# Optimization experiments

Measured on AMD Instinct MI355X. Metric: run time of the kernel, lower is better.

## Reference

```python
import jax, jax.numpy as jnp
import numpy as np

H = 8          # num_heads
L = 256        # lifting_dim
DH = L // H    # head dim


def setup_inputs() -> dict:
    key = jax.random.key(0)
    ks = jax.random.split(key, 32)
    B, N, E = 4, 16384, 65536
    Dn, De, Dg = 128, 64, 32

    def lin_w(k, din, dout):
        return jax.random.normal(k, (din, dout), jnp.float32) * (din ** -0.5)

    inp = {
        "node_features": jax.random.normal(ks[0], (B, N, Dn), jnp.float32),
        "edge_features": jax.random.normal(ks[1], (B, E, De), jnp.float32),
        "energy": jax.random.normal(ks[2], (Dg,), jnp.float32),
        "W_node": lin_w(ks[3], Dn, L), "b_node": jnp.zeros((L,), jnp.float32),
        "W_edge": lin_w(ks[4], De, L), "b_edge": jnp.zeros((L,), jnp.float32),
        "W_graph": lin_w(ks[5], Dg, L), "b_graph": jnp.zeros((L,), jnp.float32),
        "Wq": lin_w(ks[6], L, L), "bq": jnp.zeros((L,), jnp.float32),
        # stacked per-hetero-type key/value projections: [3, L, L]
        "Wk": jnp.stack([lin_w(ks[7 + i], L, L) for i in range(3)]),
        "bk": jnp.zeros((3, L), jnp.float32),
        "Wv": jnp.stack([lin_w(ks[10 + i], L, L) for i in range(3)]),
        "bv": jnp.zeros((3, L), jnp.float32),
        "W_out": lin_w(ks[13], L, L), "b_out": jnp.zeros((L,), jnp.float32),
    }
    return inp


def _heads(x, B, T):
    # [B,T,L] -> [B,H,T,DH]
    return x.reshape(B, T, H, DH).transpose(0, 2, 1, 3)


def reference(node_features, edge_features, energy,
              W_node, b_node, W_edge, b_edge, W_graph, b_graph,
              Wq, bq, Wk, bk, Wv, bv, W_out, b_out):
    B, N, _ = node_features.shape
    lifted_nodes = node_features @ W_node + b_node            # [B,N,L]
    lifted_edges = edge_features @ W_edge + b_edge            # [B,E,L]
    lifted_graph = jnp.broadcast_to(energy, (B, 1, energy.shape[0])) @ W_graph + b_graph  # [B,1,L]

    hetero = [lifted_nodes, lifted_edges, lifted_graph]

    q = _heads(lifted_nodes @ Wq + bq, B, N)                  # [B,H,N,DH]
    q = jax.nn.softmax(q, axis=-1)

    out = None
    # NOTE: faithful to the original, `out` is overwritten each iteration,
    # so only the last hetero feature (graph) determines the output.
    for i in range(3):
        h = hetero[i]
        T = h.shape[1]
        k = jax.nn.softmax(_heads(h @ Wk[i] + bk[i], B, T), axis=-1)  # [B,H,T,DH]
        v = _heads(h @ Wv[i] + bv[i], B, T)                           # [B,H,T,DH]
        k_sum = k.sum(axis=-2, keepdims=True)                          # [B,H,1,DH]
        d_inv = 1.0 / jnp.clip((q * k_sum).sum(axis=-1, keepdims=True), 1e-8)  # [B,H,N,1]
        kv = jnp.einsum("bhtd,bhte->bhde", k, v)                       # [B,H,DH,DH]
        out = q + jnp.einsum("bhnd,bhde->bhne", q, kv) * d_inv         # [B,H,N,DH]

    out = out.transpose(0, 2, 1, 3).reshape(B, N, L)
    return out @ W_out + b_out
```

## Files before the change

kernel.cpp:

```cpp
#include <hip/hip_runtime.h>
#include <hip/hip_bf16.h>
#include <cstdint>
#include <cstddef>


typedef __attribute__((ext_vector_type(8))) short short8;
typedef __attribute__((ext_vector_type(4))) short short4v;
typedef __attribute__((ext_vector_type(4))) float floatx4;

using bf16 = __hip_bfloat16;

static constexpr int Mrows = 65536;
static constexpr int Lcols = 256;

static __device__ __forceinline__ short f2bs(float x) {
  bf16 h = __float2bfloat16(x);
  return *reinterpret_cast<short*>(&h);
}

__global__ void k_setup(const float* __restrict__ W_node,
                        const float* __restrict__ Wq,
                        const float* __restrict__ W_out,
                        const float* __restrict__ energy,
                        const float* __restrict__ W_graph,
                        const float* __restrict__ b_graph,
                        const float* __restrict__ Wk,
                        const float* __restrict__ bk,
                        const float* __restrict__ Wv,
                        const float* __restrict__ bv,
                        const float* __restrict__ b_node,
                        const float* __restrict__ bq,
                        short* __restrict__ wnq_t,
                        short* __restrict__ wto_t,
                        float* __restrict__ vvec,
                        float* __restrict__ bnq) {
  const int b = blockIdx.x;
  const int t = threadIdx.x;

  if (b < 256) {
    __shared__ float wqc[256];
    const int j = b;
    wqc[t] = Wq[t * 256 + j];
    __syncthreads();
    if (t < 128) {
      const float* wr = W_node + t * 256;
      float acc = 0.f;
#pragma unroll 8
      for (int l = 0; l < 256; ++l) acc += wr[l] * wqc[l];
      wnq_t[j * 128 + t] = f2bs(acc);
    }
  } else if (b < 512) {
    const int r = b - 256;
    wto_t[t * 256 + r] = f2bs(W_out[r * 256 + t]);
  } else {
    __shared__ float ev[32];
    __shared__ float lg[256];
    __shared__ float r1[256], r2[256];
    const int h = b - 512;
    if (t < 32) ev[t] = energy[t];
    __syncthreads();

    {
      float lgd = b_graph[t];
#pragma unroll
      for (int e = 0; e < 32; ++e) lgd += ev[e] * W_graph[e * 256 + t];
      lg[t] = lgd;
    }
    __syncthreads();

    const int g = t >> 5;
    const int c = t & 31;
    const int j = h * 32 + c;
    float p1 = 0.f, p2 = 0.f;
#pragma unroll
    for (int i = 0; i < 32; ++i) {
      const int d = g * 32 + i;
      p1 += lg[d] * Wv[2 * 65536 + d * 256 + j];
      p2 += b_node[d] * Wq[d * 256 + j];
    }
    r1[t] = p1; r2[t] = p2;
    __syncthreads();
    if (t < 32) {
      float s1 = 0.f, s2 = 0.f;
#pragma unroll
      for (int gg = 0; gg < 8; ++gg) {
        s1 += r1[gg * 32 + c]; s2 += r2[gg * 32 + c];
      }
      vvec[j] = s1 + bv[512 + j];
      bnq[j]  = s2 + bq[j];
    }
  }
}

__global__ __launch_bounds__(256, 2)
void k_fused(const float* __restrict__ nf,
             const short* __restrict__ wnq,
             const short* __restrict__ wto,
             const float* __restrict__ bnq,
             const float* __restrict__ vvec,
             const float* __restrict__ b_out,
             float* __restrict__ out) {
  constexpr int AS_STR = 136;
  constexpr int PS_STR = 264;
  constexpr int FO_STR = 260;
  __shared__ short smem[64 * PS_STR];
  float* fsm = (float*)smem;

  const int t = threadIdx.x;
  const int lane = t & 63;
  const int l15 = lane & 15;
  const int lhi = lane >> 4;
  const int cw = (t >> 6) * 64;
  const int rowBase = blockIdx.x * 64;
  const int colq = cw + lhi * 4;

  const short* wb1 = wnq + (cw + l15) * 128 + lhi * 8;
  const short* wb2 = wto + (cw + l15) * 256 + lhi * 8;

  {
    const int row = t >> 2;
    const int c0 = (t & 3) << 5;
    const float* src = nf + (size_t)(rowBase + row) * 128 + c0;
    short tmp[32];
#pragma unroll
    for (int i = 0; i < 8; ++i) {
      float4 f = *(const float4*)(src + i * 4);
      tmp[i * 4 + 0] = f2bs(f.x); tmp[i * 4 + 1] = f2bs(f.y);
      tmp[i * 4 + 2] = f2bs(f.z); tmp[i * 4 + 3] = f2bs(f.w);
    }
#pragma unroll
    for (int i = 0; i < 4; ++i)
      *(short8*)(&smem[row * AS_STR + c0 + i * 8]) = *(short8*)(&tmp[i * 8]);
  }

  short8 pbf1[4][4];
#pragma unroll
  for (int kc = 0; kc < 4; ++kc)
#pragma unroll
    for (int n = 0; n < 4; ++n)
      pbf1[kc][n] = *(const short8*)(wb1 + n * 16 * 128 + kc * 32);

  __syncthreads();

  floatx4 acc[4][4];
#pragma unroll
  for (int m = 0; m < 4; ++m)
#pragma unroll
    for (int n = 0; n < 4; ++n) acc[m][n] = (floatx4){0.f, 0.f, 0.f, 0.f};

  {
#pragma unroll
    for (int kc = 0; kc < 4; ++kc) {
      short8 af[4];
#pragma unroll
      for (int m = 0; m < 4; ++m)
        af[m] = *(const short8*)(&smem[(m * 16 + l15) * AS_STR + kc * 32 + lhi * 8]);
#pragma unroll
      for (int m = 0; m < 4; ++m)
#pragma unroll
        for (int n = 0; n < 4; ++n)
          acc[m][n] = __builtin_amdgcn_mfma_f32_16x16x32_bf16(pbf1[kc][n], af[m],
                                                              acc[m][n], 0, 0, 0);
    }
  }

  short8 pbf2[2][4];
#pragma unroll
  for (int kc = 0; kc < 2; ++kc)
#pragma unroll
    for (int n = 0; n < 4; ++n)
      pbf2[kc][n] = *(const short8*)(wb2 + n * 16 * 256 + kc * 32);
  floatx4 bnq4[4], vv4[4];
#pragma unroll
  for (int n = 0; n < 4; ++n) {
    bnq4[n] = *(const floatx4*)(&bnq[colq + n * 16]);
    vv4[n]  = *(const floatx4*)(&vvec[colq + n * 16]);
  }

  __syncthreads();

#pragma unroll
  for (int m = 0; m < 4; ++m) {
#pragma unroll
    for (int tt = 0; tt < 2; ++tt) {
      const int n0 = 2 * tt, n1 = n0 + 1;
      float e0[4], e1[4];
#pragma unroll
      for (int r = 0; r < 4; ++r) {
        e0[r] = __expf(acc[m][n0][r] + bnq4[n0][r]);
        e1[r] = __expf(acc[m][n1][r] + bnq4[n1][r]);
      }
      float s = ((e0[0] + e0[1]) + (e0[2] + e0[3]))
              + ((e1[0] + e1[1]) + (e1[2] + e1[3]));
      s += __shfl_xor(s, 16);
      s += __shfl_xor(s, 32);
      const float inv = 1.0f / s;
      short4v p0, p1;
#pragma unroll
      for (int r = 0; r < 4; ++r) {
        p0[r] = f2bs(e0[r] * inv + vv4[n0][r]);
        p1[r] = f2bs(e1[r] * inv + vv4[n1][r]);
      }
      const int prow = (m * 16 + l15) * PS_STR;
      *(short4v*)(&smem[prow + colq + n0 * 16]) = p0;
      *(short4v*)(&smem[prow + colq + n1 * 16]) = p1;
    }
  }
  floatx4 bo4[4];
#pragma unroll
  for (int n = 0; n < 4; ++n) bo4[n] = *(const floatx4*)(&b_out[colq + n * 16]);
#pragma unroll
  for (int m = 0; m < 4; ++m)
#pragma unroll
    for (int n = 0; n < 4; ++n) acc[m][n] = bo4[n];
  __syncthreads();

  {
#pragma unroll
    for (int kc = 0; kc < 8; ++kc) {
      short8 af[4], bfv[4];
#pragma unroll
      for (int n = 0; n < 4; ++n)
        bfv[n] = (kc < 2) ? pbf2[kc][n]
                          : *(const short8*)(wb2 + n * 16 * 256 + kc * 32);
#pragma unroll
      for (int m = 0; m < 4; ++m)
        af[m] = *(const short8*)(&smem[(m * 16 + l15) * PS_STR + kc * 32 + lhi * 8]);
#pragma unroll
      for (int m = 0; m < 4; ++m)
#pragma unroll
        for (int n = 0; n < 4; ++n)
          acc[m][n] = __builtin_amdgcn_mfma_f32_16x16x32_bf16(bfv[n], af[m],
                                                              acc[m][n], 0, 0, 0);
    }
  }

#pragma unroll
  for (int c = 0; c < 2; ++c) {
    __syncthreads();
#pragma unroll
    for (int mm = 0; mm < 2; ++mm) {
      const int m = c * 2 + mm;
      const int frow = (mm * 16 + l15) * FO_STR;
#pragma unroll
      for (int n = 0; n < 4; ++n)
        *(floatx4*)(&fsm[frow + colq + n * 16]) = acc[m][n];
    }
    __syncthreads();
#pragma unroll
    for (int i = 0; i < 8; ++i) {
      const int f = i * 256 + t;
      const int row = f >> 6;
      const int c4 = (f & 63) << 2;
      float4 vv = *(const float4*)(&fsm[row * FO_STR + c4]);
      *(float4*)(&out[(size_t)(rowBase + c * 32 + row) * Lcols + c4]) = vv;
    }
  }
}

extern "C" void kernel_launch(void* const* d_in, const int* in_sizes, int n_in,
                              void* d_out, int out_size, void* d_ws, size_t ws_size,
                              hipStream_t stream) {
  const float* node_features = (const float*)d_in[0];
  const float* energy  = (const float*)d_in[2];
  const float* W_node  = (const float*)d_in[3];
  const float* b_node  = (const float*)d_in[4];
  const float* W_graph = (const float*)d_in[7];
  const float* b_graph = (const float*)d_in[8];
  const float* Wq      = (const float*)d_in[9];
  const float* bq      = (const float*)d_in[10];
  const float* Wk      = (const float*)d_in[11];
  const float* bk      = (const float*)d_in[12];
  const float* Wv      = (const float*)d_in[13];
  const float* bv      = (const float*)d_in[14];
  const float* W_out   = (const float*)d_in[15];
  const float* b_out   = (const float*)d_in[16];

  char* ws = (char*)d_ws;
  short* wnq_t = (short*)(ws);
  short* wto_t = (short*)(ws + 65536);
  float* vvec  = (float*)(ws + 196608);
  float* bnq   = (float*)(ws + 197632);

  k_setup<<<dim3(520), dim3(256), 0, stream>>>(
      W_node, Wq, W_out, energy, W_graph, b_graph, Wk, bk, Wv, bv,
      b_node, bq, wnq_t, wto_t, vvec, bnq);

  k_fused<<<dim3(Mrows / 64), dim3(256), 0, stream>>>(
      node_features, wnq_t, wto_t, bnq, vvec, b_out, (float*)d_out);
}
```

Measured before the change: 185.8 us.

## Process two row tiles per block with register prefetch of next tile

Each block now handles two 64-row tiles instead of one, so the grid is halved. The weight fragments and bias vectors are loaded once per block and reused across both tiles. While the current tile is computed, the next tile's node features are prefetched into registers and written to a separate shared buffer. This targets per-block setup cost and global load latency, at the cost of more registers and shared memory, which may reduce occupancy, and fewer blocks to spread across the compute units.

After: 186.3 us. No clear change (+0.3%).

```diff
diff --git a/kernel.cpp b/kernel.cpp
--- a/kernel.cpp
+++ b/kernel.cpp
@@ -12,6 +12,7 @@
 
 static constexpr int Mrows = 65536;
 static constexpr int Lcols = 256;
+static constexpr int TILES = 2;
 
 static __device__ __forceinline__ short f2bs(float x) {
   bf16 h = __float2bfloat16(x);
@@ -103,24 +104,28 @@
   constexpr int AS_STR = 136;
   constexpr int PS_STR = 264;
   constexpr int FO_STR = 260;
-  __shared__ short smem[64 * PS_STR];
-  float* fsm = (float*)smem;
+  constexpr int ASH = 64 * AS_STR;
+  __shared__ short smem[ASH + 64 * PS_STR];
+  short* als = smem;
+  short* psm = smem + ASH;
+  float* fsm = (float*)psm;
 
   const int t = threadIdx.x;
   const int lane = t & 63;
   const int l15 = lane & 15;
   const int lhi = lane >> 4;
   const int cw = (t >> 6) * 64;
-  const int rowBase = blockIdx.x * 64;
   const int colq = cw + lhi * 4;
+  const int tileBase = blockIdx.x * (TILES * 64);
+
+  const int row4 = t >> 2;
+  const int c04  = (t & 3) << 5;
 
   const short* wb1 = wnq + (cw + l15) * 128 + lhi * 8;
   const short* wb2 = wto + (cw + l15) * 256 + lhi * 8;
 
   {
-    const int row = t >> 2;
-    const int c0 = (t & 3) << 5;
-    const float* src = nf + (size_t)(rowBase + row) * 128 + c0;
+    const float* src = nf + (size_t)(tileBase + row4) * 128 + c04;
     short tmp[32];
 #pragma unroll
     for (int i = 0; i < 8; ++i) {
@@ -130,7 +135,7 @@
     }
 #pragma unroll
     for (int i = 0; i < 4; ++i)
-      *(short8*)(&smem[row * AS_STR + c0 + i * 8]) = *(short8*)(&tmp[i * 8]);
+      *(short8*)(&als[row4 * AS_STR + c04 + i * 8]) = *(short8*)(&tmp[i * 8]);
   }
 
   short8 pbf1[4][4];
@@ -139,22 +144,39 @@
 #pragma unroll
     for (int n = 0; n < 4; ++n)
       pbf1[kc][n] = *(const short8*)(wb1 + n * 16 * 128 + kc * 32);
-
-  __syncthreads();
-
-  floatx4 acc[4][4];
-#pragma unroll
-  for (int m = 0; m < 4; ++m)
-#pragma unroll
-    for (int n = 0; n < 4; ++n) acc[m][n] = (floatx4){0.f, 0.f, 0.f, 0.f};
-
-  {
+  floatx4 bnq4[4], vv4[4], bo4[4];
+#pragma unroll
+  for (int n = 0; n < 4; ++n) {
+    bnq4[n] = *(const floatx4*)(&bnq[colq + n * 16]);
+    vv4[n]  = *(const floatx4*)(&vvec[colq + n * 16]);
+    bo4[n]  = *(const floatx4*)(&b_out[colq + n * 16]);
+  }
+
+#pragma unroll
+  for (int tile = 0; tile < TILES; ++tile) {
+    const int rowBase = tileBase + tile * 64;
+
+    __syncthreads();
+
+    float4 areg[8];
+    if (tile + 1 < TILES) {
+      const float* src = nf + (size_t)(rowBase + 64 + row4) * 128 + c04;
+#pragma unroll
+      for (int i = 0; i < 8; ++i) areg[i] = *(const float4*)(src + i * 4);
+    }
+
+    floatx4 acc[4][4];
+#pragma unroll
+    for (int m = 0; m < 4; ++m)
+#pragma unroll
+      for (int n = 0; n < 4; ++n) acc[m][n] = (floatx4){0.f, 0.f, 0.f, 0.f};
+
 #pragma unroll
     for (int kc = 0; kc < 4; ++kc) {
       short8 af[4];
 #pragma unroll
       for (int m = 0; m < 4; ++m)
-        af[m] = *(const short8*)(&smem[(m * 16 + l15) * AS_STR + kc * 32 + lhi * 8]);
+        af[m] = *(const short8*)(&als[(m * 16 + l15) * AS_STR + kc * 32 + lhi * 8]);
 #pragma unroll
       for (int m = 0; m < 4; ++m)
 #pragma unroll
@@ -162,60 +184,60 @@
           acc[m][n] = __builtin_amdgcn_mfma_f32_16x16x32_bf16(pbf1[kc][n], af[m],
                                                               acc[m][n], 0, 0, 0);
     }
-  }
-
-  short8 pbf2[2][4];
-#pragma unroll
-  for (int kc = 0; kc < 2; ++kc)
-#pragma unroll
-    for (int n = 0; n < 4; ++n)
-      pbf2[kc][n] = *(const short8*)(wb2 + n * 16 * 256 + kc * 32);
-  floatx4 bnq4[4], vv4[4];
-#pragma unroll
-  for (int n = 0; n < 4; ++n) {
-    bnq4[n] = *(const floatx4*)(&bnq[colq + n * 16]);
-    vv4[n]  = *(const floatx4*)(&vvec[colq + n * 16]);
-  }
-
-  __syncthreads();
-
-#pragma unroll
-  for (int m = 0; m < 4; ++m) {
-#pragma unroll
-    for (int tt = 0; tt < 2; ++tt) {
-      const int n0 = 2 * tt, n1 = n0 + 1;
-      float e0[4], e1[4];
-#pragma unroll
-      for (int r = 0; r < 4; ++r) {
-        e0[r] = __expf(acc[m][n0][r] + bnq4[n0][r]);
-        e1[r] = __expf(acc[m][n1][r] + bnq4[n1][r]);
-      }
-      float s = ((e0[0] + e0[1]) + (e0[2] + e0[3]))
-              + ((e1[0] + e1[1]) + (e1[2] + e1[3]));
-      s += __shfl_xor(s, 16);
-      s += __shfl_xor(s, 32);
-      const float inv = 1.0f / s;
-      short4v p0, p1;
-#pragma unroll
-      for (int r = 0; r < 4; ++r) {
-        p0[r] = f2bs(e0[r] * inv + vv4[n0][r]);
-        p1[r] = f2bs(e1[r] * inv + vv4[n1][r]);
-      }
-      const int prow = (m * 16 + l15) * PS_STR;
-      *(short4v*)(&smem[prow + colq + n0 * 16]) = p0;
-      *(short4v*)(&smem[prow + colq + n1 * 16]) = p1;
-    }
-  }
-  floatx4 bo4[4];
-#pragma unroll
-  for (int n = 0; n < 4; ++n) bo4[n] = *(const floatx4*)(&b_out[colq + n * 16]);
-#pragma unroll
-  for (int m = 0; m < 4; ++m)
-#pragma unroll
-    for (int n = 0; n < 4; ++n) acc[m][n] = bo4[n];
-  __syncthreads();
-
-  {
+
+    short8 pbf2[2][4];
+#pragma unroll
+    for (int kc = 0; kc < 2; ++kc)
+#pragma unroll
+      for (int n = 0; n < 4; ++n)
+        pbf2[kc][n] = *(const short8*)(wb2 + n * 16 * 256 + kc * 32);
+
+#pragma unroll
+    for (int m = 0; m < 4; ++m) {
+#pragma unroll
+      for (int tt = 0; tt < 2; ++tt) {
+        const int n0 = 2 * tt, n1 = n0 + 1;
+        float e0[4], e1[4];
+#pragma unroll
+        for (int r = 0; r < 4; ++r) {
+          e0[r] = __expf(acc[m][n0][r] + bnq4[n0][r]);
+          e1[r] = __expf(acc[m][n1][r] + bnq4[n1][r]);
+        }
+        float s = ((e0[0] + e0[1]) + (e0[2] + e0[3]))
+                + ((e1[0] + e1[1]) + (e1[2] + e1[3]));
+        s += __shfl_xor(s, 16);
+        s += __shfl_xor(s, 32);
+        const float inv = 1.0f / s;
+        short4v p0, p1;
+#pragma unroll
+        for (int r = 0; r < 4; ++r) {
+          p0[r] = f2bs(e0[r] * inv + vv4[n0][r]);
+          p1[r] = f2bs(e1[r] * inv + vv4[n1][r]);
+        }
+        const int prow = (m * 16 + l15) * PS_STR;
+        *(short4v*)(&psm[prow + colq + n0 * 16]) = p0;
+        *(short4v*)(&psm[prow + colq + n1 * 16]) = p1;
+      }
+    }
+#pragma unroll
+    for (int m = 0; m < 4; ++m)
+#pragma unroll
+      for (int n = 0; n < 4; ++n) acc[m][n] = bo4[n];
+
+    __syncthreads();
+
+    if (tile + 1 < TILES) {
+      short tmp[32];
+#pragma unroll
+      for (int i = 0; i < 8; ++i) {
+        tmp[i * 4 + 0] = f2bs(areg[i].x); tmp[i * 4 + 1] = f2bs(areg[i].y);
+        tmp[i * 4 + 2] = f2bs(areg[i].z); tmp[i * 4 + 3] = f2bs(areg[i].w);
+      }
+#pragma unroll
+      for (int i = 0; i < 4; ++i)
+        *(short8*)(&als[row4 * AS_STR + c04 + i * 8]) = *(short8*)(&tmp[i * 8]);
+    }
+
 #pragma unroll
     for (int kc = 0; kc < 8; ++kc) {
       short8 af[4], bfv[4];
@@ -225,7 +247,7 @@
                           : *(const short8*)(wb2 + n * 16 * 256 + kc * 32);
 #pragma unroll
       for (int m = 0; m < 4; ++m)
-        af[m] = *(const short8*)(&smem[(m * 16 + l15) * PS_STR + kc * 32 + lhi * 8]);
+        af[m] = *(const short8*)(&psm[(m * 16 + l15) * PS_STR + kc * 32 + lhi * 8]);
 #pragma unroll
       for (int m = 0; m < 4; ++m)
 #pragma unroll
@@ -233,27 +255,27 @@
           acc[m][n] = __builtin_amdgcn_mfma_f32_16x16x32_bf16(bfv[n], af[m],
                                                               acc[m][n], 0, 0, 0);
     }
-  }
-
-#pragma unroll
-  for (int c = 0; c < 2; ++c) {
-    __syncthreads();
-#pragma unroll
-    for (int mm = 0; mm < 2; ++mm) {
-      const int m = c * 2 + mm;
-      const int frow = (mm * 16 + l15) * FO_STR;
-#pragma unroll
-      for (int n = 0; n < 4; ++n)
-        *(floatx4*)(&fsm[frow + colq + n * 16]) = acc[m][n];
-    }
-    __syncthreads();
-#pragma unroll
-    for (int i = 0; i < 8; ++i) {
-      const int f = i * 256 + t;
-      const int row = f >> 6;
-      const int c4 = (f & 63) << 2;
-      float4 vv = *(const float4*)(&fsm[row * FO_STR + c4]);
-      *(float4*)(&out[(size_t)(rowBase + c * 32 + row) * Lcols + c4]) = vv;
+
+#pragma unroll
+    for (int c = 0; c < 2; ++c) {
+      __syncthreads();
+#pragma unroll
+      for (int mm = 0; mm < 2; ++mm) {
+        const int m = c * 2 + mm;
+        const int frow = (mm * 16 + l15) * FO_STR;
+#pragma unroll
+        for (int n = 0; n < 4; ++n)
+          *(floatx4*)(&fsm[frow + colq + n * 16]) = acc[m][n];
+      }
+      __syncthreads();
+#pragma unroll
+      for (int i = 0; i < 8; ++i) {
+        const int f = i * 256 + t;
+        const int rr = f >> 6;
+        const int c4 = (f & 63) << 2;
+        float4 vv = *(const float4*)(&fsm[rr * FO_STR + c4]);
+        *(float4*)(&out[(size_t)(rowBase + c * 32 + rr) * Lcols + c4]) = vv;
+      }
     }
   }
 }
@@ -286,6 +308,6 @@
       W_node, Wq, W_out, energy, W_graph, b_graph, Wk, bk, Wv, bv,
       b_node, bq, wnq_t, wto_t, vvec, bnq);
 
-  k_fused<<<dim3(Mrows / 64), dim3(256), 0, stream>>>(
+  k_fused<<<dim3(Mrows / (TILES * 64)), dim3(256), 0, stream>>>(
       node_features, wnq_t, wto_t, bnq, vvec, b_out, (float*)d_out);
 }
```
